# Optimization experiments

Hardware: AMD Instinct MI355X
Metric: run time of the kernel (lower is better)

## Reference

```python
import jax, jax.numpy as jnp
import numpy as np

N_HEADS = 16
THETA = 10000.0


def _rope(x, cos, sin):
    # x: [B,H,S,hd]; pairs are interleaved (x[...,2i], x[...,2i+1]) = complex pair
    xe = x[..., 0::2]
    xo = x[..., 1::2]
    re = xe * cos - xo * sin
    im = xe * sin + xo * cos
    return jnp.stack([re, im], axis=-1).reshape(x.shape)


def setup_inputs() -> dict:
    key = jax.random.key(0)
    k1, k2, k3 = jax.random.split(key, 3)
    B, S, D = 2, 2048, 2048
    x = jax.random.normal(k1, (B, S, D), dtype=jnp.float32)
    Wqkv = jax.random.normal(k2, (D, 3 * D), dtype=jnp.float32) * (D ** -0.5)
    Wo = jax.random.normal(k3, (D, D), dtype=jnp.float32) * (D ** -0.5)
    return {"x": x, "Wqkv": Wqkv, "Wo": Wo}


def reference(x, Wqkv, Wo):
    B, S, D = x.shape
    H = N_HEADS
    hd = D // H
    half = hd // 2

    qkv = x @ Wqkv                                   # [B,S,3D]
    q, k, v = jnp.split(qkv, 3, axis=-1)
    # [B,S,D] -> [B,H,S,hd]
    q = q.reshape(B, S, H, hd).transpose(0, 2, 1, 3)
    k = k.reshape(B, S, H, hd).transpose(0, 2, 1, 3)
    v = v.reshape(B, S, H, hd).transpose(0, 2, 1, 3)

    # RoPE frequencies: thetas = theta^(-2i/hd), freqs = pos outer thetas
    i = jnp.arange(half, dtype=jnp.float32)
    inv = THETA ** (-2.0 * i / hd)
    pos = jnp.arange(S, dtype=jnp.float32)
    freqs = pos[:, None] * inv[None, :]              # [S, half]
    cos = jnp.cos(freqs)[None, None]                 # [1,1,S,half]
    sin = jnp.sin(freqs)[None, None]
    q = _rope(q, cos, sin)
    k = _rope(k, cos, sin)

    scale = 1.0 / jnp.sqrt(jnp.float32(hd))
    scores = jnp.einsum("bhqd,bhkd->bhqk", q, k) * scale
    causal = jnp.tril(jnp.ones((S, S), dtype=bool))
    scores = jnp.where(causal[None, None], scores, -jnp.inf)
    attn = jax.nn.softmax(scores, axis=-1)
    y = jnp.einsum("bhqk,bhkd->bhqd", attn, v)       # [B,H,S,hd]
    y = y.transpose(0, 2, 1, 3).reshape(B, S, D)
    return y @ Wo
```

## Files before the change

kernel.cpp:

```cpp
#include <hip/hip_runtime.h>
#include <hip/hip_bf16.h>

typedef __attribute__((ext_vector_type(4))) float f32x4;
typedef __attribute__((ext_vector_type(8))) short s16x8;
typedef unsigned short u16;
typedef unsigned int u32;

#define MFMA16 __builtin_amdgcn_mfma_f32_16x16x32_bf16

#define GLL16(g, l)                                                        \
  __builtin_amdgcn_global_load_lds(                                        \
      (const __attribute__((address_space(1))) void*)(g),                  \
      (__attribute__((address_space(3))) void*)(l), 16, 0, 0)

__device__ __forceinline__ u16 f2b(float f) {
  u32 x = __builtin_bit_cast(u32, f);
  u32 r = (x + 0x7fffu + ((x >> 16) & 1u)) >> 16;
  return (u16)r;
}
__device__ __forceinline__ float b2f(u16 u) {
  u32 x = ((u32)u) << 16;
  return __builtin_bit_cast(float, x);
}

__global__ __launch_bounds__(256) void k_cvt(const float* __restrict__ in, u16* __restrict__ out) {
  size_t i = ((size_t)blockIdx.x * 256 + threadIdx.x) * 4;
  float4 v = *(const float4*)(in + i);
  ushort4 o; o.x = f2b(v.x); o.y = f2b(v.y); o.z = f2b(v.z); o.w = f2b(v.w);
  *(ushort4*)(out + i) = o;
}

__global__ __launch_bounds__(256) void k_tconv(const float* __restrict__ in, u16* __restrict__ out,
                                               int R, int C) {
  __shared__ u16 tile[64][72];
  int c0 = blockIdx.x * 64, r0 = blockIdx.y * 64;
  int t = threadIdx.x;
#pragma unroll
  for (int p = 0; p < 4; ++p) {
    int idx = p * 1024 + t * 4;
    int row = idx >> 6, col = idx & 63;
    float4 v = *(const float4*)&in[(size_t)(r0 + row) * C + c0 + col];
    tile[row][col]     = f2b(v.x);
    tile[row][col + 1] = f2b(v.y);
    tile[row][col + 2] = f2b(v.z);
    tile[row][col + 3] = f2b(v.w);
  }
  __syncthreads();
#pragma unroll
  for (int p = 0; p < 4; ++p) {
    int idx = p * 1024 + t * 4;
    int row = idx >> 6, col = idx & 63;
    ushort4 o;
    o.x = tile[col][row]; o.y = tile[col + 1][row];
    o.z = tile[col + 2][row]; o.w = tile[col + 3][row];
    *(ushort4*)&out[(size_t)(c0 + row) * R + r0 + col] = o;
  }
}

__global__ __launch_bounds__(256) void k_trv(const u16* __restrict__ v, u16* __restrict__ vt) {
  __shared__ u16 tile[64][72];
  int bh = blockIdx.z;
  int s0 = blockIdx.x * 64, d0 = blockIdx.y * 64;
  const u16* src = v + (size_t)bh * 2048 * 128;
  u16* dst = vt + (size_t)bh * 2048 * 128;
  int t = threadIdx.x;
#pragma unroll
  for (int p = 0; p < 4; ++p) {
    int idx = p * 1024 + t * 4;
    int row = idx >> 6, col = idx & 63;
    ushort4 x = *(const ushort4*)&src[(size_t)(s0 + row) * 128 + d0 + col];
    tile[row][col] = x.x; tile[row][col + 1] = x.y;
    tile[row][col + 2] = x.z; tile[row][col + 3] = x.w;
  }
  __syncthreads();
#pragma unroll
  for (int p = 0; p < 4; ++p) {
    int idx = p * 1024 + t * 4;
    int row = idx >> 6, col = idx & 63;
    ushort4 o;
    o.x = tile[col][row]; o.y = tile[col + 1][row];
    o.z = tile[col + 2][row]; o.w = tile[col + 3][row];
    *(ushort4*)&dst[(size_t)(d0 + row) * 2048 + s0 + col] = o;
  }
}

__global__ __launch_bounds__(256) void k_trig(float2* __restrict__ tab) {
  int t = blockIdx.x * 256 + threadIdx.x;
  int s = t >> 6, i = t & 63;
  float inv = expf(-(float)i * (9.210340371976184f / 64.f));
  float a = (float)s * inv;
  float sn, cs;
  sincosf(a, &sn, &cs);
  tab[t] = make_float2(cs, sn);
}

__global__ __launch_bounds__(256) void k_rope(u16* __restrict__ q, u16* __restrict__ k,
                                              const float2* __restrict__ tab) {
  u16* ptr = blockIdx.y ? k : q;
  size_t tid = (size_t)blockIdx.x * 256 + threadIdx.x;
  int g = (int)(tid & 15);
  int s = (int)((tid >> 4) & 2047);
  int bh = (int)(tid >> 15);
  size_t base = ((size_t)bh * 2048 + s) * 128 + (size_t)g * 8;
  uint4 dv = *(const uint4*)(ptr + base);
  u16* pu = (u16*)&dv;
  const float2* tb = &tab[s * 64 + g * 4];
#pragma unroll
  for (int j = 0; j < 4; ++j) {
    float xe = b2f(pu[2 * j]), xo = b2f(pu[2 * j + 1]);
    float c = tb[j].x, sn = tb[j].y;
    pu[2 * j]     = f2b(xe * c - xo * sn);
    pu[2 * j + 1] = f2b(xe * sn + xo * c);
  }
  *(uint4*)(ptr + base) = dv;
}

__global__ __launch_bounds__(256) void k_gemm_qkv(const u16* __restrict__ A, const u16* __restrict__ Bt,
                                                  u16* __restrict__ qo, u16* __restrict__ ko,
                                                  u16* __restrict__ vo) {
  constexpr int K = 2048;
  __shared__ u16 sa[128][32];
  __shared__ u16 sb[128][32];
  int n0 = blockIdx.x * 128;
  int m0 = blockIdx.y * 128;
  int t = threadIdx.x;
  int lane = t & 63, w = t >> 6;
  int wm = (w >> 1) * 64, wn = (w & 1) * 64;
  int lr = lane & 15, lg = lane >> 4;
  int srow0 = w * 32 + (lane >> 2);
  int srow1 = srow0 + 16;
  int scol = (lane & 3) * 8;
  const u16* gA0 = &A[(size_t)(m0 + srow0) * K + scol];
  const u16* gA1 = &A[(size_t)(m0 + srow1) * K + scol];
  const u16* gB0 = &Bt[(size_t)(n0 + srow0) * K + scol];
  const u16* gB1 = &Bt[(size_t)(n0 + srow1) * K + scol];
  u16* lA0 = &sa[srow0][scol];
  u16* lA1 = &sa[srow1][scol];
  u16* lB0 = &sb[srow0][scol];
  u16* lB1 = &sb[srow1][scol];
  f32x4 acc[4][4] = {};
  for (int k0 = 0; k0 < K; k0 += 32) {
    __syncthreads();
    GLL16(gA0 + k0, lA0); GLL16(gA1 + k0, lA1);
    GLL16(gB0 + k0, lB0); GLL16(gB1 + k0, lB1);
    __syncthreads();
    s16x8 af[4], bf[4];
#pragma unroll
    for (int i = 0; i < 4; ++i) af[i] = *(const s16x8*)&sa[wm + i * 16 + lr][lg * 8];
#pragma unroll
    for (int i = 0; i < 4; ++i) bf[i] = *(const s16x8*)&sb[wn + i * 16 + lr][lg * 8];
#pragma unroll
    for (int mi = 0; mi < 4; ++mi)
#pragma unroll
      for (int ni = 0; ni < 4; ++ni)
        acc[mi][ni] = MFMA16(af[mi], bf[ni], acc[mi][ni], 0, 0, 0);
  }
  int which = blockIdx.x >> 4;
  int h = blockIdx.x & 15;
  u16* dst = which == 0 ? qo : (which == 1 ? ko : vo);
#pragma unroll
  for (int mi = 0; mi < 4; ++mi)
#pragma unroll
    for (int ni = 0; ni < 4; ++ni)
#pragma unroll
      for (int r = 0; r < 4; ++r) {
        int m = m0 + wm + mi * 16 + lg * 4 + r;
        int d = wn + ni * 16 + lr;
        int b = m >> 11, s = m & 2047;
        dst[(((size_t)b * 16 + h) * 2048 + s) * 128 + d] = f2b(acc[mi][ni][r]);
      }
}

__global__ __launch_bounds__(256) void k_gemm_out(const u16* __restrict__ A, const u16* __restrict__ Bt,
                                                  float* __restrict__ C) {
  constexpr int K = 2048, N = 2048;
  __shared__ u16 sa[128][32];
  __shared__ u16 sb[128][32];
  int n0 = blockIdx.x * 128;
  int m0 = blockIdx.y * 128;
  int t = threadIdx.x;
  int lane = t & 63, w = t >> 6;
  int wm = (w >> 1) * 64, wn = (w & 1) * 64;
  int lr = lane & 15, lg = lane >> 4;
  int srow0 = w * 32 + (lane >> 2);
  int srow1 = srow0 + 16;
  int scol = (lane & 3) * 8;
  const u16* gA0 = &A[(size_t)(m0 + srow0) * K + scol];
  const u16* gA1 = &A[(size_t)(m0 + srow1) * K + scol];
  const u16* gB0 = &Bt[(size_t)(n0 + srow0) * K + scol];
  const u16* gB1 = &Bt[(size_t)(n0 + srow1) * K + scol];
  u16* lA0 = &sa[srow0][scol];
  u16* lA1 = &sa[srow1][scol];
  u16* lB0 = &sb[srow0][scol];
  u16* lB1 = &sb[srow1][scol];
  f32x4 acc[4][4] = {};
  for (int k0 = 0; k0 < K; k0 += 32) {
    __syncthreads();
    GLL16(gA0 + k0, lA0); GLL16(gA1 + k0, lA1);
    GLL16(gB0 + k0, lB0); GLL16(gB1 + k0, lB1);
    __syncthreads();
    s16x8 af[4], bf[4];
#pragma unroll
    for (int i = 0; i < 4; ++i) af[i] = *(const s16x8*)&sa[wm + i * 16 + lr][lg * 8];
#pragma unroll
    for (int i = 0; i < 4; ++i) bf[i] = *(const s16x8*)&sb[wn + i * 16 + lr][lg * 8];
#pragma unroll
    for (int mi = 0; mi < 4; ++mi)
#pragma unroll
      for (int ni = 0; ni < 4; ++ni)
        acc[mi][ni] = MFMA16(af[mi], bf[ni], acc[mi][ni], 0, 0, 0);
  }
#pragma unroll
  for (int mi = 0; mi < 4; ++mi)
#pragma unroll
    for (int ni = 0; ni < 4; ++ni)
#pragma unroll
      for (int r = 0; r < 4; ++r) {
        int m = m0 + wm + mi * 16 + lg * 4 + r;
        int n = n0 + wn + ni * 16 + lr;
        C[(size_t)m * N + n] = acc[mi][ni][r];
      }
}

__global__ __launch_bounds__(256) void k_attn(const u16* __restrict__ q, const u16* __restrict__ k,
                                              const u16* __restrict__ vt, u16* __restrict__ y) {
  constexpr int S = 2048, HD = 128;
  __shared__ u16 kt[2][64][128];
  __shared__ u16 vtl[2][128][64];
  __shared__ u16 pl[4][16][72];
  int bh = blockIdx.x;
  int qt = (gridDim.y - 1) - blockIdx.y;
  int q0 = qt * 64;
  int t = threadIdx.x, lane = t & 63, w = t >> 6;
  int lr = lane & 15, lg = lane >> 4;
  const size_t base = (size_t)bh * S * HD;
  const u16* kbh = k + base;
  const u16* vbh = vt + base;

  int kr_l = ((w * 4) << 2) + (lane >> 4);
  int kcb_base = (lane & 15) << 4;
  int vr_l = ((w * 4) << 3) + (lane >> 3);
  int vcb_base = (lane & 7) << 4;

  s16x8 aq[4];
  {
    size_t qrow = base + (size_t)(q0 + w * 16 + lr) * HD;
#pragma unroll
    for (int i = 0; i < 4; ++i) aq[i] = *(const s16x8*)&q[qrow + i * 32 + lg * 8];
  }
  f32x4 o[8] = {};
  float mrow[4] = {-INFINITY, -INFINITY, -INFINITY, -INFINITY};
  float lsum[4] = {};
  const float scale = 0.08838834764831845f;
  int kv_end = q0 + 64;

#define STAGE_KV(buf, kv)                                                             \
  {                                                                                   \
    _Pragma("unroll")                                                                 \
    for (int i = 0; i < 4; ++i) {                                                     \
      int kr = kr_l + 4 * i;                                                          \
      int kcb = kcb_base ^ ((kr & 7) << 4);                                           \
      GLL16((const char*)(kbh + (size_t)((kv) + kr) * HD) + kcb,                      \
            (char*)&kt[buf][0][0] + ((w * 4 + i) << 10) + (lane << 4));               \
      int vr = vr_l + 8 * i;                                                          \
      int vcb = vcb_base ^ ((vr & 7) << 4);                                           \
      GLL16((const char*)(vbh + (size_t)vr * S + (kv)) + vcb,                         \
            (char*)&vtl[buf][0][0] + ((w * 4 + i) << 10) + (lane << 4));              \
    }                                                                                 \
  }

  STAGE_KV(0, 0);
  int cur = 0;
  for (int kv0 = 0; kv0 < kv_end; kv0 += 64) {
    __syncthreads();
    if (kv0 + 64 < kv_end) STAGE_KV(cur ^ 1, kv0 + 64);
    f32x4 sf[4] = {};
    int swz = (lr & 7) << 4;
    __builtin_amdgcn_s_setprio(1);
#pragma unroll
    for (int dstep = 0; dstep < 4; ++dstep)
#pragma unroll
      for (int nt = 0; nt < 4; ++nt) {
        int cb = ((dstep << 6) + (lg << 4)) ^ swz;
        s16x8 bk = *(const s16x8*)((const char*)&kt[cur][nt * 16 + lr][0] + cb);
        sf[nt] = MFMA16(aq[dstep], bk, sf[nt], 0, 0, 0);
      }
    __builtin_amdgcn_s_setprio(0);
    int grow0 = q0 + w * 16 + lg * 4;
    float pmax[4] = {-INFINITY, -INFINITY, -INFINITY, -INFINITY};
#pragma unroll
    for (int nt = 0; nt < 4; ++nt) {
      int col = kv0 + nt * 16 + lr;
#pragma unroll
      for (int r = 0; r < 4; ++r) {
        float sv = sf[nt][r] * scale;
        if (col > grow0 + r) sv = -INFINITY;
        sf[nt][r] = sv;
        pmax[r] = fmaxf(pmax[r], sv);
      }
    }
#pragma unroll
    for (int off = 1; off < 16; off <<= 1)
#pragma unroll
      for (int r = 0; r < 4; ++r) pmax[r] = fmaxf(pmax[r], __shfl_xor(pmax[r], off));
    float alpha[4], ps[4];
#pragma unroll
    for (int r = 0; r < 4; ++r) {
      float mn = fmaxf(mrow[r], pmax[r]);
      alpha[r] = __expf(mrow[r] - mn);
      mrow[r] = mn;
      ps[r] = 0.f;
#pragma unroll
      for (int nt = 0; nt < 4; ++nt) { float e = __expf(sf[nt][r] - mn); sf[nt][r] = e; ps[r] += e; }
    }
#pragma unroll
    for (int off = 1; off < 16; off <<= 1)
#pragma unroll
      for (int r = 0; r < 4; ++r) ps[r] += __shfl_xor(ps[r], off);
#pragma unroll
    for (int r = 0; r < 4; ++r) {
      lsum[r] = lsum[r] * alpha[r] + ps[r];
#pragma unroll
      for (int dt = 0; dt < 8; ++dt) o[dt][r] *= alpha[r];
    }
#pragma unroll
    for (int nt = 0; nt < 4; ++nt)
#pragma unroll
      for (int r = 0; r < 4; ++r)
        pl[w][lg * 4 + r][nt * 16 + lr] = f2b(sf[nt][r]);
    asm volatile("s_waitcnt lgkmcnt(0)" ::: "memory");
    __builtin_amdgcn_sched_barrier(0);
    s16x8 pa0 = *(const s16x8*)&pl[w][lr][lg * 8];
    s16x8 pa1 = *(const s16x8*)&pl[w][lr][32 + lg * 8];
    __builtin_amdgcn_s_setprio(1);
#pragma unroll
    for (int dt = 0; dt < 8; ++dt) {
      int cb0 = (lg << 4) ^ swz;
      int cb1 = (64 + (lg << 4)) ^ swz;
      s16x8 bv0 = *(const s16x8*)((const char*)&vtl[cur][dt * 16 + lr][0] + cb0);
      s16x8 bv1 = *(const s16x8*)((const char*)&vtl[cur][dt * 16 + lr][0] + cb1);
      o[dt] = MFMA16(pa0, bv0, o[dt], 0, 0, 0);
      o[dt] = MFMA16(pa1, bv1, o[dt], 0, 0, 0);
    }
    __builtin_amdgcn_s_setprio(0);
    cur ^= 1;
  }
#undef STAGE_KV
  int b = bh >> 4, h = bh & 15;
#pragma unroll
  for (int dt = 0; dt < 8; ++dt)
#pragma unroll
    for (int r = 0; r < 4; ++r) {
      int srow = q0 + w * 16 + lg * 4 + r;
      float val = o[dt][r] / lsum[r];
      y[((size_t)(b * 2048 + srow)) * 2048 + h * 128 + dt * 16 + lr] = f2b(val);
    }
}

extern "C" void kernel_launch(void* const* d_in, const int* in_sizes, int n_in,
                              void* d_out, int out_size, void* d_ws, size_t ws_size,
                              hipStream_t stream) {
  const float* x    = (const float*)d_in[0];
  const float* wqkv = (const float*)d_in[1];
  const float* wo   = (const float*)d_in[2];
  float* out = (float*)d_out;
  char* ws = (char*)d_ws;
  u16* xb    = (u16*)(ws);
  u16* wqkvt = (u16*)(ws + (size_t)(16)  * 1048576);
  u16* wot   = (u16*)(ws + (size_t)(40)  * 1048576);
  u16* qb    = (u16*)(ws + (size_t)(48)  * 1048576);
  u16* kb    = (u16*)(ws + (size_t)(64)  * 1048576);
  u16* vb    = (u16*)(ws + (size_t)(80)  * 1048576);
  u16* vtb   = (u16*)(ws + (size_t)(96)  * 1048576);
  u16* yb    = (u16*)(ws + (size_t)(112) * 1048576);
  float2* trig = (float2*)(ws + (size_t)(128) * 1048576);

  k_cvt<<<8192, 256, 0, stream>>>(x, xb);
  k_tconv<<<dim3(96, 32), 256, 0, stream>>>(wqkv, wqkvt, 2048, 6144);
  k_tconv<<<dim3(32, 32), 256, 0, stream>>>(wo, wot, 2048, 2048);
  k_trig<<<512, 256, 0, stream>>>(trig);
  k_gemm_qkv<<<dim3(48, 32), 256, 0, stream>>>(xb, wqkvt, qb, kb, vb);
  k_rope<<<dim3(4096, 2), 256, 0, stream>>>(qb, kb, trig);
  k_trv<<<dim3(32, 2, 32), 256, 0, stream>>>(vb, vtb);
  k_attn<<<dim3(32, 32), 256, 0, stream>>>(qb, kb, vtb, yb);
  k_gemm_out<<<dim3(16, 32), 256, 0, stream>>>(yb, wot, out);
}
```

Measured before the change: 299.6 us.

## Replace GEMM kernels with double-buffered 128x256 tile, 8-wave swizzled LDS kernel

Both projection GEMMs are replaced by one templated kernel using 512 threads, 128x256 output tiles, BK=64, and double-buffered LDS. The next k-tile is prefetched with global_load_lds while the current one is consumed. LDS columns are XOR-swizzled to avoid bank conflicts, and block IDs are remapped across 8 groups for better L2 locality. s_setprio and explicit waitcnt/barrier scheduling are added around the MFMA blocks. This aims to remove the sync-bound, small-K-step pipeline of the old GEMMs, at the cost of more LDS per block and lower occupancy.

```diff
diff --git a/kernel.cpp b/kernel.cpp
--- a/kernel.cpp
+++ b/kernel.cpp
@@ -115,111 +115,119 @@
   *(uint4*)(ptr + base) = dv;
 }
 
-__global__ __launch_bounds__(256) void k_gemm_qkv(const u16* __restrict__ A, const u16* __restrict__ Bt,
-                                                  u16* __restrict__ qo, u16* __restrict__ ko,
-                                                  u16* __restrict__ vo) {
+template <int MODE>
+__global__ __launch_bounds__(512) void k_gemm8(const u16* __restrict__ A, const u16* __restrict__ Bt,
+                                               u16* __restrict__ qo, u16* __restrict__ ko,
+                                               u16* __restrict__ vo, float* __restrict__ C) {
   constexpr int K = 2048;
-  __shared__ u16 sa[128][32];
-  __shared__ u16 sb[128][32];
-  int n0 = blockIdx.x * 128;
-  int m0 = blockIdx.y * 128;
-  int t = threadIdx.x;
-  int lane = t & 63, w = t >> 6;
-  int wm = (w >> 1) * 64, wn = (w & 1) * 64;
+  constexpr int NT = K / 64;
+  __shared__ u16 sA[2][128 * 64];
+  __shared__ u16 sB[2][256 * 64];
+  int tid = threadIdx.x;
+  int lane = tid & 63, w = tid >> 6;
+  int wr = w >> 2, wc = w & 3;
   int lr = lane & 15, lg = lane >> 4;
-  int srow0 = w * 32 + (lane >> 2);
-  int srow1 = srow0 + 16;
-  int scol = (lane & 3) * 8;
-  const u16* gA0 = &A[(size_t)(m0 + srow0) * K + scol];
-  const u16* gA1 = &A[(size_t)(m0 + srow1) * K + scol];
-  const u16* gB0 = &Bt[(size_t)(n0 + srow0) * K + scol];
-  const u16* gB1 = &Bt[(size_t)(n0 + srow1) * K + scol];
-  u16* lA0 = &sa[srow0][scol];
-  u16* lA1 = &sa[srow1][scol];
-  u16* lB0 = &sb[srow0][scol];
-  u16* lB1 = &sb[srow1][scol];
+
+  int id = blockIdx.y * gridDim.x + blockIdx.x;
+  int cpx = (gridDim.x * gridDim.y) >> 3;
+  int swz = (id & 7) * cpx + (id >> 3);
+  int n0 = (swz % gridDim.x) * 256;
+  int m0 = (swz / gridDim.x) * 128;
+
+  int srow = tid >> 3;
+  int swzcolb = ((tid & 7) << 4) ^ ((srow & 7) << 4);
+  const char* gA = (const char*)(A + (size_t)(m0 + srow) * K) + swzcolb;
+  const char* gB = (const char*)(Bt + (size_t)(n0 + srow) * K) + swzcolb;
+
+#define STAGE8(buf, k0)                                                      \
+  {                                                                          \
+    _Pragma("unroll") for (int rb = 0; rb < 4; ++rb)                         \
+        GLL16(gB + ((size_t)rb * 64 * K + (k0)) * 2,                         \
+              (char*)&sB[buf][0] + rb * 8192 + tid * 16);                    \
+    _Pragma("unroll") for (int ra = 0; ra < 2; ++ra)                         \
+        GLL16(gA + ((size_t)ra * 64 * K + (k0)) * 2,                         \
+              (char*)&sA[buf][0] + ra * 8192 + tid * 16);                    \
+  }
+
+  int colb0 = (lg << 4) ^ ((lr & 7) << 4);
+  int aRowByte = (wr * 64 + lr) * 128;
+  int bRowByte = (wc * 64 + lr) * 128;
+
   f32x4 acc[4][4] = {};
-  for (int k0 = 0; k0 < K; k0 += 32) {
-    __syncthreads();
-    GLL16(gA0 + k0, lA0); GLL16(gA1 + k0, lA1);
-    GLL16(gB0 + k0, lB0); GLL16(gB1 + k0, lB1);
-    __syncthreads();
+
+  STAGE8(0, 0);
+  asm volatile("s_waitcnt vmcnt(0)" ::: "memory");
+  __builtin_amdgcn_s_barrier();
+
+  for (int t = 0; t < NT; ++t) {
+    int cur = t & 1;
+    const char* sAb = (const char*)&sA[0][0] + cur * (128 * 64 * 2);
+    const char* sBb = (const char*)&sB[0][0] + cur * (256 * 64 * 2);
+    if (t + 1 < NT) STAGE8(cur ^ 1, (t + 1) * 64);
     s16x8 af[4], bf[4];
 #pragma unroll
-    for (int i = 0; i < 4; ++i) af[i] = *(const s16x8*)&sa[wm + i * 16 + lr][lg * 8];
-#pragma unroll
-    for (int i = 0; i < 4; ++i) bf[i] = *(const s16x8*)&sb[wn + i * 16 + lr][lg * 8];
+    for (int i = 0; i < 4; ++i) af[i] = *(const s16x8*)(sAb + aRowByte + i * 2048 + colb0);
+#pragma unroll
+    for (int i = 0; i < 4; ++i) bf[i] = *(const s16x8*)(sBb + bRowByte + i * 2048 + colb0);
+    __builtin_amdgcn_s_barrier();
+    asm volatile("s_waitcnt lgkmcnt(0)" ::: "memory");
+    __builtin_amdgcn_sched_barrier(0);
+    __builtin_amdgcn_s_setprio(1);
 #pragma unroll
     for (int mi = 0; mi < 4; ++mi)
 #pragma unroll
       for (int ni = 0; ni < 4; ++ni)
         acc[mi][ni] = MFMA16(af[mi], bf[ni], acc[mi][ni], 0, 0, 0);
-  }
-  int which = blockIdx.x >> 4;
-  int h = blockIdx.x & 15;
-  u16* dst = which == 0 ? qo : (which == 1 ? ko : vo);
-#pragma unroll
-  for (int mi = 0; mi < 4; ++mi)
-#pragma unroll
-    for (int ni = 0; ni < 4; ++ni)
-#pragma unroll
-      for (int r = 0; r < 4; ++r) {
-        int m = m0 + wm + mi * 16 + lg * 4 + r;
-        int d = wn + ni * 16 + lr;
-        int b = m >> 11, s = m & 2047;
-        dst[(((size_t)b * 16 + h) * 2048 + s) * 128 + d] = f2b(acc[mi][ni][r]);
-      }
-}
-
-__global__ __launch_bounds__(256) void k_gemm_out(const u16* __restrict__ A, const u16* __restrict__ Bt,
-                                                  float* __restrict__ C) {
-  constexpr int K = 2048, N = 2048;
-  __shared__ u16 sa[128][32];
-  __shared__ u16 sb[128][32];
-  int n0 = blockIdx.x * 128;
-  int m0 = blockIdx.y * 128;
-  int t = threadIdx.x;
-  int lane = t & 63, w = t >> 6;
-  int wm = (w >> 1) * 64, wn = (w & 1) * 64;
-  int lr = lane & 15, lg = lane >> 4;
-  int srow0 = w * 32 + (lane >> 2);
-  int srow1 = srow0 + 16;
-  int scol = (lane & 3) * 8;
-  const u16* gA0 = &A[(size_t)(m0 + srow0) * K + scol];
-  const u16* gA1 = &A[(size_t)(m0 + srow1) * K + scol];
-  const u16* gB0 = &Bt[(size_t)(n0 + srow0) * K + scol];
-  const u16* gB1 = &Bt[(size_t)(n0 + srow1) * K + scol];
-  u16* lA0 = &sa[srow0][scol];
-  u16* lA1 = &sa[srow1][scol];
-  u16* lB0 = &sb[srow0][scol];
-  u16* lB1 = &sb[srow1][scol];
-  f32x4 acc[4][4] = {};
-  for (int k0 = 0; k0 < K; k0 += 32) {
-    __syncthreads();
-    GLL16(gA0 + k0, lA0); GLL16(gA1 + k0, lA1);
-    GLL16(gB0 + k0, lB0); GLL16(gB1 + k0, lB1);
-    __syncthreads();
-    s16x8 af[4], bf[4];
-#pragma unroll
-    for (int i = 0; i < 4; ++i) af[i] = *(const s16x8*)&sa[wm + i * 16 + lr][lg * 8];
-#pragma unroll
-    for (int i = 0; i < 4; ++i) bf[i] = *(const s16x8*)&sb[wn + i * 16 + lr][lg * 8];
+    __builtin_amdgcn_s_setprio(0);
+    __builtin_amdgcn_s_barrier();
+#pragma unroll
+    for (int i = 0; i < 4; ++i) af[i] = *(const s16x8*)(sAb + aRowByte + i * 2048 + (colb0 ^ 64));
+#pragma unroll
+    for (int i = 0; i < 4; ++i) bf[i] = *(const s16x8*)(sBb + bRowByte + i * 2048 + (colb0 ^ 64));
+    __builtin_amdgcn_s_barrier();
+    asm volatile("s_waitcnt lgkmcnt(0)" ::: "memory");
+    __builtin_amdgcn_sched_barrier(0);
+    __builtin_amdgcn_s_setprio(1);
 #pragma unroll
     for (int mi = 0; mi < 4; ++mi)
 #pragma unroll
       for (int ni = 0; ni < 4; ++ni)
         acc[mi][ni] = MFMA16(af[mi], bf[ni], acc[mi][ni], 0, 0, 0);
-  }
-#pragma unroll
-  for (int mi = 0; mi < 4; ++mi)
-#pragma unroll
-    for (int ni = 0; ni < 4; ++ni)
-#pragma unroll
-      for (int r = 0; r < 4; ++r) {
-        int m = m0 + wm + mi * 16 + lg * 4 + r;
-        int n = n0 + wn + ni * 16 + lr;
-        C[(size_t)m * N + n] = acc[mi][ni][r];
-      }
+    __builtin_amdgcn_s_setprio(0);
+    asm volatile("s_waitcnt vmcnt(0)" ::: "memory");
+    __builtin_amdgcn_s_barrier();
+  }
+#undef STAGE8
+
+  if constexpr (MODE == 0) {
+#pragma unroll
+    for (int ni = 0; ni < 4; ++ni) {
+      int n = n0 + wc * 64 + ni * 16 + lr;
+      int which = n >> 11;
+      int h = (n >> 7) & 15;
+      int d = n & 127;
+      u16* dst = which == 0 ? qo : (which == 1 ? ko : vo);
+#pragma unroll
+      for (int mi = 0; mi < 4; ++mi)
+#pragma unroll
+        for (int r = 0; r < 4; ++r) {
+          int m = m0 + wr * 64 + mi * 16 + lg * 4 + r;
+          int b = m >> 11, s = m & 2047;
+          dst[(((size_t)b * 16 + h) * 2048 + s) * 128 + d] = f2b(acc[mi][ni][r]);
+        }
+    }
+  } else {
+#pragma unroll
+    for (int mi = 0; mi < 4; ++mi)
+#pragma unroll
+      for (int ni = 0; ni < 4; ++ni)
+#pragma unroll
+        for (int r = 0; r < 4; ++r) {
+          int m = m0 + wr * 64 + mi * 16 + lg * 4 + r;
+          int n = n0 + wc * 64 + ni * 16 + lr;
+          C[(size_t)m * 2048 + n] = acc[mi][ni][r];
+        }
+  }
 }
 
 __global__ __launch_bounds__(256) void k_attn(const u16* __restrict__ q, const u16* __restrict__ k,
@@ -379,9 +387,9 @@
   k_tconv<<<dim3(96, 32), 256, 0, stream>>>(wqkv, wqkvt, 2048, 6144);
   k_tconv<<<dim3(32, 32), 256, 0, stream>>>(wo, wot, 2048, 2048);
   k_trig<<<512, 256, 0, stream>>>(trig);
-  k_gemm_qkv<<<dim3(48, 32), 256, 0, stream>>>(xb, wqkvt, qb, kb, vb);
+  k_gemm8<0><<<dim3(24, 32), 512, 0, stream>>>(xb, wqkvt, qb, kb, vb, nullptr);
   k_rope<<<dim3(4096, 2), 256, 0, stream>>>(qb, kb, trig);
   k_trv<<<dim3(32, 2, 32), 256, 0, stream>>>(vb, vtb);
   k_attn<<<dim3(32, 32), 256, 0, stream>>>(qb, kb, vtb, yb);
-  k_gemm_out<<<dim3(16, 32), 256, 0, stream>>>(yb, wot, out);
-}
+  k_gemm8<1><<<dim3(8, 32), 512, 0, stream>>>(yb, wot, nullptr, nullptr, nullptr, out);
+}
```

After: 353.2 us. +17.9%, slower.
